# Kernel optimization log

Measured on AMD Instinct MI355X. Metric: run time of the kernel, lower is better.

Reference implementation:

```python
import jax, jax.numpy as jnp
import numpy as np

B = 128
N = 65536          # total nodes across batched subgraphs
E = 1048576        # total edges
CLIP_DIM = 768
PD = 512           # projection_dim


def setup_inputs() -> dict:
    key = jax.random.key(0)
    ks = jax.random.split(key, 20)
    s = 0.02
    return {
        # CLIP-encoded features (clip encoders treated as upstream feature extractors)
        "image_features": jax.random.normal(ks[0], (B, CLIP_DIM), jnp.float32),
        "text_features": jax.random.normal(ks[1], (B, CLIP_DIM), jnp.float32),
        "answer": jax.random.uniform(ks[2], (B,), jnp.float32),
        # batched subgraph (X_fixed rows already gathered, as in extract_subgraph_batch)
        "x_nodes": jax.random.normal(ks[3], (N, PD), jnp.float32),
        "edge_index": jax.random.randint(ks[4], (2, E), 0, N, jnp.int32),
        "batch_vec": jnp.sort(jax.random.randint(ks[5], (N,), 0, B, jnp.int32)),
        # image/text projections (clip_dim != projection_dim -> Linear)
        "W_img": jax.random.normal(ks[6], (CLIP_DIM, PD), jnp.float32) * s,
        "b_img": jnp.zeros((PD,), jnp.float32),
        "W_txt": jax.random.normal(ks[7], (CLIP_DIM, PD), jnp.float32) * s,
        "b_txt": jnp.zeros((PD,), jnp.float32),
        # implicit classifier: Linear(2*PD, PD) -> ReLU -> Linear(PD, 1)
        "W1": jax.random.normal(ks[8], (2 * PD, PD), jnp.float32) * s,
        "b1": jnp.zeros((PD,), jnp.float32),
        "W2": jax.random.normal(ks[9], (PD, 1), jnp.float32) * s,
        "b2": jnp.zeros((1,), jnp.float32),
        # GCNConv(PD, PD)
        "Wg": jax.random.normal(ks[10], (PD, PD), jnp.float32) * s,
        "bg": jnp.zeros((PD,), jnp.float32),
        # symbolic classifier: Linear(PD, PD) -> ReLU -> Linear(PD, 1)
        "Ws1": jax.random.normal(ks[11], (PD, PD), jnp.float32) * s,
        "bs1": jnp.zeros((PD,), jnp.float32),
        "Ws2": jax.random.normal(ks[12], (PD, 1), jnp.float32) * s,
        "bs2": jnp.zeros((1,), jnp.float32),
    }


def gcn_conv(x, edge_index, W, b):
    """PyG GCNConv: h = W x; add self-loops; sym-normalized sum aggregation."""
    n = x.shape[0]
    h = x @ W                                     # [N, PD] dense GEMM
    loop = jnp.arange(n, dtype=edge_index.dtype)
    src = jnp.concatenate([edge_index[0], loop])  # [E+N]
    dst = jnp.concatenate([edge_index[1], loop])
    deg = jax.ops.segment_sum(jnp.ones_like(dst, dtype=h.dtype), dst, num_segments=n)
    dis = jax.lax.rsqrt(deg)                      # deg >= 1 (self loops)
    norm = dis[src] * dis[dst]                    # [E+N]
    out = jax.ops.segment_sum(h[src] * norm[:, None], dst, num_segments=n)
    return out + b


def reference(image_features, text_features, answer, x_nodes, edge_index, batch_vec,
              W_img, b_img, W_txt, b_txt, W1, b1, W2, b2,
              Wg, bg, Ws1, bs1, Ws2, bs2):
    # ---- implicit branch (MedicalVQAModel.forward) ----
    img = image_features @ W_img + b_img          # [B, PD]
    txt = text_features @ W_txt + b_txt           # [B, PD]
    combined = jnp.concatenate([img, txt], axis=-1)
    h = jax.nn.relu(combined @ W1 + b1)           # dropout p=0.1 inactive (eval)
    y_implicit = (h @ W2 + b2)[:, 0]              # [B]

    # ---- symbolic branch: GCN over batched subgraphs ----
    x = gcn_conv(x_nodes, edge_index, Wg, bg)
    x = jax.nn.relu(x)                            # dropout p=0.8 inactive (eval)
    bv = batch_vec.astype(jnp.int32)
    sums = jax.ops.segment_sum(x, bv, num_segments=B)          # [B, PD]
    cnts = jax.ops.segment_sum(jnp.ones((x.shape[0],), x.dtype), bv, num_segments=B)
    graph_features = sums / jnp.maximum(cnts, 1.0)[:, None]    # global_mean_pool
    hs = jax.nn.relu(graph_features @ Ws1 + bs1)
    y_symbolic = (hs @ Ws2 + bs2)[:, 0]           # [B]

    logits = jnp.maximum(y_implicit, y_symbolic)
    # BCEWithLogits (mean): log(1+e^l) - l*y
    loss = jnp.mean(jnp.logaddexp(0.0, logits) - logits * answer)
    return (logits, loss)
```

## Files before the change

### kernel.cpp

```cpp
#include <hip/hip_runtime.h>
#include <stdint.h>

#define N_NODES 65536
#define N_EDGES 1048576
#define BATCH   128
#define PD      512
#define CLIPD   768

typedef __attribute__((ext_vector_type(4))) float f32x4;
typedef __attribute__((ext_vector_type(2))) float f32x2;
typedef __attribute__((ext_vector_type(4))) int   i32x4;

__device__ __forceinline__ unsigned short f2b(float f) {
    uint32_t u = __float_as_uint(f);
    return (unsigned short)((u + 0x7fffu + ((u >> 16) & 1u)) >> 16);
}

__global__ void k_wgt(const float* __restrict__ Wg, unsigned short* __restrict__ WgT,
                      const int* __restrict__ bv, int* __restrict__ cnts) {
    __shared__ float tile[32][33];
    int kb = blockIdx.x * 32, nb = blockIdx.y * 32;
    int tx = threadIdx.x, ty = threadIdx.y;
    if (kb == 0 && nb == 0) {
        int tid = ty * 32 + tx;
        if (tid < BATCH) {
            int lo = 0, hi = N_NODES;
            while (lo < hi) { int m = (lo + hi) >> 1; if (bv[m] < tid) lo = m + 1; else hi = m; }
            int lo2 = lo, hi2 = N_NODES;
            while (lo2 < hi2) { int m = (lo2 + hi2) >> 1; if (bv[m] < tid + 1) lo2 = m + 1; else hi2 = m; }
            cnts[tid] = lo2 - lo;
        }
    }
    tile[ty][tx] = Wg[(size_t)(kb + ty) * PD + nb + tx];
    __syncthreads();
    WgT[(size_t)(nb + ty) * PD + kb + tx] = f2b(tile[tx][ty]);
}

__global__ void k_init(int* __restrict__ deg, int* __restrict__ fill,
                       float* __restrict__ sums) {
    int i = blockIdx.x * 256 + threadIdx.x;
    deg[i] = 1;
    fill[i] = 0;
    sums[i] = 0.f;
}

__global__ void k_deg(const int* __restrict__ ei, int* __restrict__ deg) {
    int e = blockIdx.x * 256 + threadIdx.x;
    atomicAdd(&deg[ei[N_EDGES + e]], 1);
}

__global__ void k_scan(const int* __restrict__ deg, int* __restrict__ row_ptr,
                       float* __restrict__ dis) {
    __shared__ int wsum[16];
    const int t = threadIdx.x;
    const int w = t >> 6, l = t & 63;
    const int base = w * 4096;
    int s = 0;
    for (int i = 0; i < 64; ++i) s += deg[base + i * 64 + l];
    s -= 64;
#pragma unroll
    for (int off = 1; off < 64; off <<= 1) s += __shfl_xor(s, off);
    if (l == 0) wsum[w] = s;
    __syncthreads();
    int carry = 0;
    for (int i = 0; i < 16; ++i) carry += (i < w) ? wsum[i] : 0;
    int idx = base + l;
    int d = deg[idx];
    for (int i = 0; i < 64; ++i) {
        int dn = 0;
        if (i < 63) dn = deg[idx + 64];
        int v = d - 1;
        int inc = v;
#pragma unroll
        for (int off = 1; off < 64; off <<= 1) {
            int n = __shfl_up(inc, off);
            if (l >= off) inc += n;
        }
        row_ptr[idx] = carry + inc - v;
        dis[idx] = rsqrtf((float)d);
        carry += __shfl(inc, 63);
        idx += 64;
        d = dn;
    }
    if (t == 1023) row_ptr[N_NODES] = carry;
}

__global__ void k_scatter(const int* __restrict__ ei, const int* __restrict__ row_ptr,
                          int* __restrict__ fill, int* __restrict__ srcs) {
    int e = blockIdx.x * 256 + threadIdx.x;
    int d = ei[N_EDGES + e];
    int pos = row_ptr[d] + atomicAdd(&fill[d], 1);
    srcs[pos] = ei[e];
}

__device__ __forceinline__ void mfma16(f32x4& acc, i32x4 a, i32x4 b) {
    asm("v_mfma_f32_16x16x32_bf16 %0, %1, %2, %0" : "+v"(acc) : "v"(a), "v"(b));
}

__global__ __launch_bounds__(256) void k_gemm(const float* __restrict__ X,
                                              const unsigned short* __restrict__ WgT,
                                              const float* __restrict__ dis,
                                              uint8_t* __restrict__ hn8) {
    __shared__ __align__(16) unsigned short As[128 * 32];
    __shared__ __align__(16) unsigned short Bs[256 * 32];
    const int m0 = blockIdx.x * 128;
    const int n0 = blockIdx.y * 256;
    const int t = threadIdx.x;
    const int lane = t & 63, w = t >> 6;
    const int wr = w >> 1, wc = w & 1;
    const int g = lane >> 4, lr = lane & 15;

    f32x4 acc[4][8] = {};

    for (int k0 = 0; k0 < PD; k0 += 32) {
        __syncthreads();
#pragma unroll
        for (int it = 0; it < 4; ++it) {
            int idx = it * 256 + t;
            int r = idx >> 3, kc = (idx & 7) * 4;
            float4 v = *(const float4*)&X[(size_t)(m0 + r) * PD + k0 + kc];
            uint2 o;
            o.x = (uint32_t)f2b(v.x) | ((uint32_t)f2b(v.y) << 16);
            o.y = (uint32_t)f2b(v.z) | ((uint32_t)f2b(v.w) << 16);
            *(uint2*)&As[r * 32 + kc] = o;
        }
#pragma unroll
        for (int it = 0; it < 4; ++it) {
            int idx = it * 256 + t;
            int r = idx >> 2, kc = (idx & 3) * 8;
            *(uint4*)&Bs[r * 32 + kc] = *(const uint4*)&WgT[(size_t)(n0 + r) * PD + k0 + kc];
        }
        __syncthreads();

        i32x4 a[4], b[8];
#pragma unroll
        for (int i = 0; i < 4; ++i) a[i] = *(const i32x4*)&As[(wr * 64 + i * 16 + lr) * 32 + g * 8];
#pragma unroll
        for (int j = 0; j < 8; ++j) b[j] = *(const i32x4*)&Bs[(wc * 128 + j * 16 + lr) * 32 + g * 8];
#pragma unroll
        for (int i = 0; i < 4; ++i)
#pragma unroll
            for (int j = 0; j < 8; ++j) mfma16(acc[i][j], a[i], b[j]);
    }
    asm volatile("s_nop 7\n s_nop 7\n s_nop 7\n s_nop 7");

#pragma unroll
    for (int i = 0; i < 4; ++i) {
#pragma unroll
        for (int r = 0; r < 4; ++r) {
            int row = m0 + wr * 64 + i * 16 + g * 4 + r;
            float dd = dis[row];
#pragma unroll
            for (int j = 0; j < 8; ++j) {
                int col = n0 + wc * 128 + j * 16 + lr;
                float val = acc[i][j][r] * dd;
                uint32_t p = __builtin_amdgcn_cvt_pk_fp8_f32(val, val, 0, false);
                hn8[(size_t)row * PD + col] = (uint8_t)p;
            }
        }
    }
}

#define NPW 8
__device__ __forceinline__ void acc8(float a[8], uint2 v) {
    f32x2 l0 = __builtin_amdgcn_cvt_pk_f32_fp8(v.x, false);
    f32x2 h0 = __builtin_amdgcn_cvt_pk_f32_fp8(v.x, true);
    f32x2 l1 = __builtin_amdgcn_cvt_pk_f32_fp8(v.y, false);
    f32x2 h1 = __builtin_amdgcn_cvt_pk_f32_fp8(v.y, true);
    a[0] += l0[0]; a[1] += l0[1]; a[2] += h0[0]; a[3] += h0[1];
    a[4] += l1[0]; a[5] += l1[1]; a[6] += h1[0]; a[7] += h1[1];
}

__global__ __launch_bounds__(256) void k_agg(const uint8_t* __restrict__ hn8,
                                             const float* __restrict__ dis,
                                             const float* __restrict__ bg,
                                             const int* __restrict__ row_ptr,
                                             const int* __restrict__ srcs,
                                             const int* __restrict__ bv,
                                             float* __restrict__ sums) {
    const int t = threadIdx.x;
    const int w = t >> 6, lane = t & 63;
    const int c0 = lane * 8;
    const int node0 = (blockIdx.x * 4 + w) * NPW;
    float bgv[8];
#pragma unroll
    for (int j = 0; j < 8; ++j) bgv[j] = bg[c0 + j];
    float s[8] = {};
    int curb = bv[node0];
    for (int ni = 0; ni < NPW; ++ni) {
        int node = node0 + ni;
        int b = bv[node];
        if (b != curb) {
#pragma unroll
            for (int j = 0; j < 8; ++j) atomicAdd(&sums[(size_t)curb * PD + c0 + j], s[j]);
#pragma unroll
            for (int j = 0; j < 8; ++j) s[j] = 0.f;
            curb = b;
        }
        float a[8] = {};
        int beg = row_ptr[node], end = row_ptr[node + 1];
        int e = beg;
        for (; e + 8 <= end; e += 8) {
            int sn[8];
#pragma unroll
            for (int q = 0; q < 8; ++q) sn[q] = srcs[e + q];
            uint2 v[8];
#pragma unroll
            for (int q = 0; q < 8; ++q)
                v[q] = *(const uint2*)&hn8[(size_t)sn[q] * PD + c0];
#pragma unroll
            for (int q = 0; q < 8; ++q) acc8(a, v[q]);
        }
        for (; e < end; ++e) {
            uint2 v = *(const uint2*)&hn8[(size_t)srcs[e] * PD + c0];
            acc8(a, v);
        }
        {
            uint2 v = *(const uint2*)&hn8[(size_t)node * PD + c0];
            acc8(a, v);
        }
        float dd = dis[node];
#pragma unroll
        for (int j = 0; j < 8; ++j) {
            float r = fmaxf(fmaf(a[j], dd, bgv[j]), 0.f);
            s[j] += r;
        }
    }
#pragma unroll
    for (int j = 0; j < 8; ++j) atomicAdd(&sums[(size_t)curb * PD + c0 + j], s[j]);
}

__device__ __forceinline__ void lin_part_core(const float* __restrict__ a,
                                              const float* __restrict__ wp,
                                              float* __restrict__ P, int slot, int c0) {
    float acc0 = 0.f, acc1 = 0.f, acc2 = 0.f, acc3 = 0.f;
    float acc4 = 0.f, acc5 = 0.f, acc6 = 0.f, acc7 = 0.f;
#pragma unroll 4
    for (int k = 0; k < 256; k += 8) {
        float a0 = a[k + 0], a1 = a[k + 1], a2 = a[k + 2], a3 = a[k + 3];
        float a4 = a[k + 4], a5 = a[k + 5], a6 = a[k + 6], a7 = a[k + 7];
        float2 w0 = *(const float2*)&wp[(size_t)(k + 0) * PD];
        float2 w1 = *(const float2*)&wp[(size_t)(k + 1) * PD];
        float2 w2 = *(const float2*)&wp[(size_t)(k + 2) * PD];
        float2 w3 = *(const float2*)&wp[(size_t)(k + 3) * PD];
        float2 w4 = *(const float2*)&wp[(size_t)(k + 4) * PD];
        float2 w5 = *(const float2*)&wp[(size_t)(k + 5) * PD];
        float2 w6 = *(const float2*)&wp[(size_t)(k + 6) * PD];
        float2 w7 = *(const float2*)&wp[(size_t)(k + 7) * PD];
        acc0 = fmaf(a0, w0.x, acc0); acc1 = fmaf(a0, w0.y, acc1);
        acc2 = fmaf(a1, w1.x, acc2); acc3 = fmaf(a1, w1.y, acc3);
        acc4 = fmaf(a2, w2.x, acc4); acc5 = fmaf(a2, w2.y, acc5);
        acc6 = fmaf(a3, w3.x, acc6); acc7 = fmaf(a3, w3.y, acc7);
        acc0 = fmaf(a4, w4.x, acc0); acc1 = fmaf(a4, w4.y, acc1);
        acc2 = fmaf(a5, w5.x, acc2); acc3 = fmaf(a5, w5.y, acc3);
        acc4 = fmaf(a6, w6.x, acc4); acc5 = fmaf(a6, w6.y, acc5);
        acc6 = fmaf(a7, w7.x, acc6); acc7 = fmaf(a7, w7.y, acc7);
    }
    P[(size_t)slot * PD + c0] = (acc0 + acc2) + (acc4 + acc6);
    P[(size_t)slot * PD + c0 + 1] = (acc1 + acc3) + (acc5 + acc7);
}

__global__ __launch_bounds__(256) void k_lin_part(const float* __restrict__ A,
                                                  const float* __restrict__ W,
                                                  float* __restrict__ P, int K) {
    const int row = blockIdx.x, kc = blockIdx.y, c0 = threadIdx.x * 2;
    lin_part_core(A + (size_t)row * K + kc * 256, W + (size_t)kc * 256 * PD + c0,
                  P, row * 8 + kc, c0);
}

__global__ __launch_bounds__(256) void k_lin_part_it(const float* __restrict__ IMG,
                                                     const float* __restrict__ TXT,
                                                     const float* __restrict__ Wi,
                                                     const float* __restrict__ Wt,
                                                     float* __restrict__ P) {
    const int row = blockIdx.x, kc = blockIdx.y, c0 = threadIdx.x * 2;
    const float* A = (kc < 3) ? IMG : TXT;
    const float* W = (kc < 3) ? Wi : Wt;
    const int sub = (kc < 3) ? kc : kc - 3;
    lin_part_core(A + (size_t)row * CLIPD + sub * 256, W + (size_t)sub * 256 * PD + c0,
                  P, row * 8 + kc, c0);
}

__global__ __launch_bounds__(256) void k_lin_red_it(const float* __restrict__ P,
                                                    const float* __restrict__ bi,
                                                    const float* __restrict__ bt,
                                                    float* __restrict__ C) {
    const int row = blockIdx.x, side = blockIdx.y, c0 = threadIdx.x * 2;
    const float* p = P + ((size_t)row * 8 + side * 3) * PD + c0;
    float r0 = p[0] + p[PD] + p[2 * PD];
    float r1 = p[1] + p[PD + 1] + p[2 * PD + 1];
    const float* bias = side ? bt : bi;
    C[(size_t)row * 1024 + side * PD + c0] = r0 + bias[c0];
    C[(size_t)row * 1024 + side * PD + c0 + 1] = r1 + bias[c0 + 1];
}

__global__ __launch_bounds__(256) void k_reddot(const float* __restrict__ P,
                                                const float* __restrict__ bias,
                                                const float* __restrict__ w2,
                                                const float* __restrict__ b2,
                                                float* __restrict__ y,
                                                int nch, const int* __restrict__ cnts) {
    __shared__ float wred[4];
    const int row = blockIdx.x;
    const int t = threadIdx.x;
    const int c0 = t * 2;
    const float* p = P + (size_t)row * 8 * PD + c0;
    float r0 = p[0], r1 = p[1];
    if (nch > 1) { r0 += p[PD];     r1 += p[PD + 1]; }
    if (nch > 2) { r0 += p[2 * PD]; r1 += p[2 * PD + 1]; }
    if (nch > 3) { r0 += p[3 * PD]; r1 += p[3 * PD + 1]; }
    float s = 1.f;
    if (cnts) s = 1.f / fmaxf((float)cnts[row], 1.f);
    r0 = fmaxf(fmaf(r0, s, bias[c0]), 0.f);
    r1 = fmaxf(fmaf(r1, s, bias[c0 + 1]), 0.f);
    float partial = fmaf(r0, w2[c0], r1 * w2[c0 + 1]);
#pragma unroll
    for (int off = 32; off; off >>= 1) partial += __shfl_down(partial, off);
    if ((t & 63) == 0) wred[t >> 6] = partial;
    __syncthreads();
    if (t == 0) y[row] = (wred[0] + wred[1]) + (wred[2] + wred[3]) + b2[0];
}

__global__ void k_final(const float* __restrict__ yi, const float* __restrict__ ys,
                        const float* __restrict__ ans, float* __restrict__ out) {
    __shared__ float red[128];
    int t = threadIdx.x;
    float l = fmaxf(yi[t], ys[t]);
    out[t] = l;
    float li = fmaxf(l, 0.f) + log1pf(expf(-fabsf(l))) - l * ans[t];
    red[t] = li;
    __syncthreads();
    for (int off = 64; off; off >>= 1) {
        if (t < off) red[t] += red[t + off];
        __syncthreads();
    }
    if (t == 0) out[BATCH] = red[0] / (float)BATCH;
}

extern "C" void kernel_launch(void* const* d_in, const int* in_sizes, int n_in,
                              void* d_out, int out_size, void* d_ws, size_t ws_size,
                              hipStream_t stream) {
    const float* image_features = (const float*)d_in[0];
    const float* text_features  = (const float*)d_in[1];
    const float* answer         = (const float*)d_in[2];
    const float* x_nodes        = (const float*)d_in[3];
    const int*   edge_index     = (const int*)d_in[4];
    const int*   batch_vec      = (const int*)d_in[5];
    const float* W_img = (const float*)d_in[6];
    const float* b_img = (const float*)d_in[7];
    const float* W_txt = (const float*)d_in[8];
    const float* b_txt = (const float*)d_in[9];
    const float* W1  = (const float*)d_in[10];
    const float* b1  = (const float*)d_in[11];
    const float* W2  = (const float*)d_in[12];
    const float* b2  = (const float*)d_in[13];
    const float* Wg  = (const float*)d_in[14];
    const float* bg  = (const float*)d_in[15];
    const float* Ws1 = (const float*)d_in[16];
    const float* bs1 = (const float*)d_in[17];
    const float* Ws2 = (const float*)d_in[18];
    const float* bs2 = (const float*)d_in[19];
    float* out = (float*)d_out;

    char* base = (char*)d_ws;
    size_t cur = 0;
    auto alloc = [&](size_t bytes) -> void* {
        void* r = base + cur;
        cur = (cur + bytes + 255) & ~(size_t)255;
        return r;
    };
    unsigned short* WgT = (unsigned short*)alloc((size_t)PD * PD * 2);
    uint8_t* hn8   = (uint8_t*)alloc((size_t)N_NODES * PD);
    int*   deg     = (int*)alloc((size_t)N_NODES * 4);
    float* dis     = (float*)alloc((size_t)N_NODES * 4);
    int*   row_ptr = (int*)alloc((size_t)(N_NODES + 1) * 4);
    int*   fill    = (int*)alloc((size_t)N_NODES * 4);
    int*   srcs    = (int*)alloc((size_t)N_EDGES * 4);
    float* sums    = (float*)alloc((size_t)BATCH * PD * 4);
    int*   cnts    = (int*)alloc((size_t)BATCH * 4);
    float* Ppart   = (float*)alloc((size_t)BATCH * 8 * PD * 4);
    float* combined = (float*)alloc((size_t)BATCH * 1024 * 4);
    float* yi      = (float*)alloc((size_t)BATCH * 4);
    float* ys      = (float*)alloc((size_t)BATCH * 4);

    hipLaunchKernelGGL(k_wgt, dim3(16, 16), dim3(32, 32), 0, stream, Wg, WgT, batch_vec, cnts);
    hipLaunchKernelGGL(k_init, dim3(256), dim3(256), 0, stream, deg, fill, sums);
    hipLaunchKernelGGL(k_deg, dim3(4096), dim3(256), 0, stream, edge_index, deg);
    hipLaunchKernelGGL(k_scan, dim3(1), dim3(1024), 0, stream, deg, row_ptr, dis);
    hipLaunchKernelGGL(k_scatter, dim3(4096), dim3(256), 0, stream, edge_index, row_ptr, fill, srcs);
    hipLaunchKernelGGL(k_gemm, dim3(N_NODES / 128, PD / 256), dim3(256), 0, stream,
                       x_nodes, WgT, dis, hn8);
    hipLaunchKernelGGL(k_agg, dim3(N_NODES / (NPW * 4)), dim3(256), 0, stream,
                       hn8, dis, bg, row_ptr, srcs, batch_vec, sums);

    hipLaunchKernelGGL(k_lin_part_it, dim3(BATCH, 6), dim3(256), 0, stream,
                       image_features, text_features, W_img, W_txt, Ppart);
    hipLaunchKernelGGL(k_lin_red_it, dim3(BATCH, 2), dim3(256), 0, stream,
                       Ppart, b_img, b_txt, combined);
    hipLaunchKernelGGL(k_lin_part, dim3(BATCH, 4), dim3(256), 0, stream,
                       combined, W1, Ppart, 1024);
    hipLaunchKernelGGL(k_reddot, dim3(BATCH), dim3(256), 0, stream,
                       Ppart, b1, W2, b2, yi, 4, (const int*)nullptr);

    hipLaunchKernelGGL(k_lin_part, dim3(BATCH, 2), dim3(256), 0, stream,
                       sums, Ws1, Ppart, PD);
    hipLaunchKernelGGL(k_reddot, dim3(BATCH), dim3(256), 0, stream,
                       Ppart, bs1, Ws2, bs2, ys, 2, cnts);

    hipLaunchKernelGGL(k_final, dim3(1), dim3(128), 0, stream, yi, ys, answer, out);
}
```

Baseline: 442.0 us.

## Spread aggregation channels across a full block per node group and memset buffers

The aggregation kernel changes its mapping. Before, each wave handled 8 nodes with each lane covering 8 channels through 8-byte gathers. Now a 256-thread block covers the 512 channels, each thread handling 2 channels with 2-byte gathers, and the edge loop unrolls to 16. This gives more blocks and more outstanding gathers per node, at the cost of narrower memory accesses and more instructions per byte. Separately, the init kernel is replaced by memsets and the degree count starts at 0, with the self-loop folded into the scan.

Measured after the change: 383.1 us. 13.3% less time.

```diff
diff --git a/kernel.cpp b/kernel.cpp
--- a/kernel.cpp
+++ b/kernel.cpp
@@ -36,14 +36,6 @@
     WgT[(size_t)(nb + ty) * PD + kb + tx] = f2b(tile[tx][ty]);
 }
 
-__global__ void k_init(int* __restrict__ deg, int* __restrict__ fill,
-                       float* __restrict__ sums) {
-    int i = blockIdx.x * 256 + threadIdx.x;
-    deg[i] = 1;
-    fill[i] = 0;
-    sums[i] = 0.f;
-}
-
 __global__ void k_deg(const int* __restrict__ ei, int* __restrict__ deg) {
     int e = blockIdx.x * 256 + threadIdx.x;
     atomicAdd(&deg[ei[N_EDGES + e]], 1);
@@ -57,7 +49,6 @@
     const int base = w * 4096;
     int s = 0;
     for (int i = 0; i < 64; ++i) s += deg[base + i * 64 + l];
-    s -= 64;
 #pragma unroll
     for (int off = 1; off < 64; off <<= 1) s += __shfl_xor(s, off);
     if (l == 0) wsum[w] = s;
@@ -69,7 +60,7 @@
     for (int i = 0; i < 64; ++i) {
         int dn = 0;
         if (i < 63) dn = deg[idx + 64];
-        int v = d - 1;
+        int v = d;
         int inc = v;
 #pragma unroll
         for (int off = 1; off < 64; off <<= 1) {
@@ -77,7 +68,7 @@
             if (l >= off) inc += n;
         }
         row_ptr[idx] = carry + inc - v;
-        dis[idx] = rsqrtf((float)d);
+        dis[idx] = rsqrtf((float)(d + 1));
         carry += __shfl(inc, 63);
         idx += 64;
         d = dn;
@@ -161,16 +152,7 @@
     }
 }
 
-#define NPW 8
-__device__ __forceinline__ void acc8(float a[8], uint2 v) {
-    f32x2 l0 = __builtin_amdgcn_cvt_pk_f32_fp8(v.x, false);
-    f32x2 h0 = __builtin_amdgcn_cvt_pk_f32_fp8(v.x, true);
-    f32x2 l1 = __builtin_amdgcn_cvt_pk_f32_fp8(v.y, false);
-    f32x2 h1 = __builtin_amdgcn_cvt_pk_f32_fp8(v.y, true);
-    a[0] += l0[0]; a[1] += l0[1]; a[2] += h0[0]; a[3] += h0[1];
-    a[4] += l1[0]; a[5] += l1[1]; a[6] += h1[0]; a[7] += h1[1];
-}
-
+#define NPB 8
 __global__ __launch_bounds__(256) void k_agg(const uint8_t* __restrict__ hn8,
                                              const float* __restrict__ dis,
                                              const float* __restrict__ bg,
@@ -179,55 +161,72 @@
                                              const int* __restrict__ bv,
                                              float* __restrict__ sums) {
     const int t = threadIdx.x;
-    const int w = t >> 6, lane = t & 63;
-    const int c0 = lane * 8;
-    const int node0 = (blockIdx.x * 4 + w) * NPW;
-    float bgv[8];
-#pragma unroll
-    for (int j = 0; j < 8; ++j) bgv[j] = bg[c0 + j];
-    float s[8] = {};
+    const int c0 = t * 2;
+    const int node0 = blockIdx.x * NPB;
+    const float bg0 = bg[c0], bg1 = bg[c0 + 1];
+    float s0 = 0.f, s1 = 0.f;
     int curb = bv[node0];
-    for (int ni = 0; ni < NPW; ++ni) {
+    for (int ni = 0; ni < NPB; ++ni) {
         int node = node0 + ni;
         int b = bv[node];
         if (b != curb) {
-#pragma unroll
-            for (int j = 0; j < 8; ++j) atomicAdd(&sums[(size_t)curb * PD + c0 + j], s[j]);
-#pragma unroll
-            for (int j = 0; j < 8; ++j) s[j] = 0.f;
+            atomicAdd(&sums[(size_t)curb * PD + c0], s0);
+            atomicAdd(&sums[(size_t)curb * PD + c0 + 1], s1);
+            s0 = s1 = 0.f;
             curb = b;
         }
-        float a[8] = {};
+        float a0 = 0.f, a1 = 0.f;
         int beg = row_ptr[node], end = row_ptr[node + 1];
         int e = beg;
+        for (; e + 16 <= end; e += 16) {
+            int sn[16];
+#pragma unroll
+            for (int q = 0; q < 16; ++q) sn[q] = srcs[e + q];
+            uint32_t v[16];
+#pragma unroll
+            for (int q = 0; q < 16; ++q)
+                v[q] = *(const unsigned short*)&hn8[(size_t)sn[q] * PD + c0];
+#pragma unroll
+            for (int q = 0; q < 16; ++q) {
+                f32x2 f = __builtin_amdgcn_cvt_pk_f32_fp8(v[q], false);
+                a0 += f[0];
+                a1 += f[1];
+            }
+        }
         for (; e + 8 <= end; e += 8) {
             int sn[8];
 #pragma unroll
             for (int q = 0; q < 8; ++q) sn[q] = srcs[e + q];
-            uint2 v[8];
+            uint32_t v[8];
 #pragma unroll
             for (int q = 0; q < 8; ++q)
-                v[q] = *(const uint2*)&hn8[(size_t)sn[q] * PD + c0];
-#pragma unroll
-            for (int q = 0; q < 8; ++q) acc8(a, v[q]);
+                v[q] = *(const unsigned short*)&hn8[(size_t)sn[q] * PD + c0];
+#pragma unroll
+            for (int q = 0; q < 8; ++q) {
+                f32x2 f = __builtin_amdgcn_cvt_pk_f32_fp8(v[q], false);
+                a0 += f[0];
+                a1 += f[1];
+            }
         }
         for (; e < end; ++e) {
-            uint2 v = *(const uint2*)&hn8[(size_t)srcs[e] * PD + c0];
-            acc8(a, v);
-        }
-        {
-            uint2 v = *(const uint2*)&hn8[(size_t)node * PD + c0];
-            acc8(a, v);
-        }
+            int sn = srcs[e];
+            uint32_t v = *(const unsigned short*)&hn8[(size_t)sn * PD + c0];
+            f32x2 f = __builtin_amdgcn_cvt_pk_f32_fp8(v, false);
+            a0 += f[0];
+            a1 += f[1];
+        }
+        uint32_t v = *(const unsigned short*)&hn8[(size_t)node * PD + c0];
+        f32x2 f = __builtin_amdgcn_cvt_pk_f32_fp8(v, false);
+        a0 += f[0];
+        a1 += f[1];
         float dd = dis[node];
-#pragma unroll
-        for (int j = 0; j < 8; ++j) {
-            float r = fmaxf(fmaf(a[j], dd, bgv[j]), 0.f);
-            s[j] += r;
-        }
-    }
-#pragma unroll
-    for (int j = 0; j < 8; ++j) atomicAdd(&sums[(size_t)curb * PD + c0 + j], s[j]);
+        a0 = fmaxf(fmaf(a0, dd, bg0), 0.f);
+        a1 = fmaxf(fmaf(a1, dd, bg1), 0.f);
+        s0 += a0;
+        s1 += a1;
+    }
+    atomicAdd(&sums[(size_t)curb * PD + c0], s0);
+    atomicAdd(&sums[(size_t)curb * PD + c0 + 1], s1);
 }
 
 __device__ __forceinline__ void lin_part_core(const float* __restrict__ a,
@@ -383,14 +382,17 @@
     float* yi      = (float*)alloc((size_t)BATCH * 4);
     float* ys      = (float*)alloc((size_t)BATCH * 4);
 
+    hipMemsetAsync(deg, 0, (size_t)N_NODES * 4, stream);
+    hipMemsetAsync(fill, 0, (size_t)N_NODES * 4, stream);
+    hipMemsetAsync(sums, 0, (size_t)BATCH * PD * 4, stream);
+
     hipLaunchKernelGGL(k_wgt, dim3(16, 16), dim3(32, 32), 0, stream, Wg, WgT, batch_vec, cnts);
-    hipLaunchKernelGGL(k_init, dim3(256), dim3(256), 0, stream, deg, fill, sums);
     hipLaunchKernelGGL(k_deg, dim3(4096), dim3(256), 0, stream, edge_index, deg);
     hipLaunchKernelGGL(k_scan, dim3(1), dim3(1024), 0, stream, deg, row_ptr, dis);
     hipLaunchKernelGGL(k_scatter, dim3(4096), dim3(256), 0, stream, edge_index, row_ptr, fill, srcs);
     hipLaunchKernelGGL(k_gemm, dim3(N_NODES / 128, PD / 256), dim3(256), 0, stream,
                        x_nodes, WgT, dis, hn8);
-    hipLaunchKernelGGL(k_agg, dim3(N_NODES / (NPW * 4)), dim3(256), 0, stream,
+    hipLaunchKernelGGL(k_agg, dim3(N_NODES / NPB), dim3(256), 0, stream,
                        hn8, dis, bg, row_ptr, srcs, batch_vec, sums);
 
     hipLaunchKernelGGL(k_lin_part_it, dim3(BATCH, 6), dim3(256), 0, stream,
```
